# Kernel tuning notes

Hardware: AMD Instinct MI355X
Metric: run time of the kernel (lower is better)

The kernel has to match this reference:

```python
import jax, jax.numpy as jnp
import numpy as np

N_NODES = 100000
N_EDGES = 3200000
N_GRAPHS = 64
NEG_SLOPE = 0.2


def mish(x):
    return x * jnp.tanh(jax.nn.softplus(x))


def gat_layer(x, src, dst, W, b, a_src, a_dst, heads, out_ch, n_nodes):
    # h: [N, H, C]
    h = (x @ W).reshape(n_nodes, heads, out_ch)
    alpha_s = jnp.sum(h * a_src[None], axis=-1)  # [N, H]
    alpha_d = jnp.sum(h * a_dst[None], axis=-1)  # [N, H]
    e = jax.nn.leaky_relu(alpha_s[src] + alpha_d[dst], NEG_SLOPE)  # [E, H]
    # scatter-softmax over incoming edges of each destination node
    emax = jax.ops.segment_max(e, dst, num_segments=n_nodes)  # [N, H]
    ee = jnp.exp(e - emax[dst])
    den = jax.ops.segment_sum(ee, dst, num_segments=n_nodes)
    alpha = ee / (den[dst] + 1e-16)  # [E, H]
    msg = h[src] * alpha[..., None]  # [E, H, C]
    out = jax.ops.segment_sum(msg, dst, num_segments=n_nodes)
    return out.reshape(n_nodes, heads * out_ch) + b


def setup_inputs() -> dict:
    key = jax.random.key(0)
    ks = jax.random.split(key, 10)
    x = jax.random.normal(ks[0], (N_NODES, 128), dtype=jnp.float32)
    edge_index = jax.random.randint(ks[1], (2, N_EDGES), 0, N_NODES, dtype=jnp.int64)
    batch = jnp.sort(jax.random.randint(ks[2], (N_NODES,), 0, N_GRAPHS, dtype=jnp.int64))
    s1 = 1.0 / np.sqrt(128.0)
    s2 = 1.0 / np.sqrt(16.0)
    return {
        "x": x,
        "edge_index": edge_index,
        "batch": batch,
        "W1": jax.random.normal(ks[3], (128, 16), dtype=jnp.float32) * s1,
        "b1": jnp.zeros((16,), dtype=jnp.float32),
        "a_src1": jax.random.normal(ks[4], (4, 4), dtype=jnp.float32) * 0.5,
        "a_dst1": jax.random.normal(ks[5], (4, 4), dtype=jnp.float32) * 0.5,
        "W2": jax.random.normal(ks[6], (16, 32), dtype=jnp.float32) * s2,
        "b2": jnp.zeros((32,), dtype=jnp.float32),
        "a_src2": jax.random.normal(ks[7], (1, 32), dtype=jnp.float32) * 0.5,
        "a_dst2": jax.random.normal(ks[8], (1, 32), dtype=jnp.float32) * 0.5,
    }


def reference(x, edge_index, batch, W1, b1, a_src1, a_dst1, W2, b2, a_src2, a_dst2):
    n = x.shape[0]
    # PyG GATConv default add_self_loops=True
    loop = jnp.arange(n, dtype=edge_index.dtype)
    src = jnp.concatenate([edge_index[0], loop])
    dst = jnp.concatenate([edge_index[1], loop])
    h = mish(gat_layer(x, src, dst, W1, b1, a_src1, a_dst1, heads=4, out_ch=4, n_nodes=n))
    h = mish(gat_layer(h, src, dst, W2, b2, a_src2, a_dst2, heads=1, out_ch=32, n_nodes=n))
    # global_mean_pool
    sums = jax.ops.segment_sum(h, batch, num_segments=N_GRAPHS)
    cnts = jax.ops.segment_sum(jnp.ones((n,), h.dtype), batch, num_segments=N_GRAPHS)
    return sums / jnp.maximum(cnts, 1.0)[:, None]
```

## Files before the change

### kernel.cpp

```cpp
#include <hip/hip_runtime.h>
#include <hip/hip_fp16.h>
#include <math.h>

#define NEG_SLOPE 0.2f
#define GB 192
#define SB 256
#define NBMAX 1024
#define CAP 5120
#define CAPH 2560

typedef _Float16 half2v __attribute__((ext_vector_type(2)));
typedef _Float16 half4v __attribute__((ext_vector_type(4)));

__device__ __forceinline__ float mishf(float x) {
    if (x > 15.f) return x;
    float ex = __expf(x);
    float y = 1.f + ex;
    float y2 = y * y;
    return x * (y2 - 1.f) / (y2 + 1.f);
}

__device__ __forceinline__ float lw(float e) {
    return __expf(fmaxf(e, NEG_SLOPE * e));
}

__device__ __forceinline__ float hdot2a(half2v a, half2v b, float c) {
#if __has_builtin(__builtin_amdgcn_fdot2)
    return __builtin_amdgcn_fdot2(a, b, c, false);
#else
    return (float)a.x * (float)b.x + (float)a.y * (float)b.y + c;
#endif
}

__global__ __launch_bounds__(1024) void front_kernel(
        const float* __restrict__ x, const float* __restrict__ W1,
        const float* __restrict__ a_dst,
        const float* __restrict__ W2, const float* __restrict__ as2,
        const float* __restrict__ ad2,
        _Float16* __restrict__ hpre1h, float* __restrict__ addst,
        float* __restrict__ vs, float* __restrict__ vd,
        const int* __restrict__ src, const int* __restrict__ dst,
        int E, int Etot, int CH, int NB, int N, int NT,
        int* __restrict__ cursor, int* __restrict__ pairs) {
    __shared__ __attribute__((aligned(16))) char smem[42240];
    int tid = threadIdx.x;
    if (blockIdx.x < GB) {
        float* Wlt = (float*)smem;
        float* xs  = Wlt + 16 * 132;
        if (blockIdx.x == 0 && tid < 16) {
            float ps = 0.f, pd = 0.f;
            #pragma unroll
            for (int c = 0; c < 32; c++) {
                float w = W2[tid * 32 + c];
                ps += w * as2[c];
                pd += w * ad2[c];
            }
            vs[tid] = ps; vd[tid] = pd;
        }
        for (int i = tid; i < 2048; i += 1024) Wlt[(i & 15) * 132 + (i >> 4)] = W1[i];
        int nl = tid >> 4, ch = tid & 15;
        for (int t = blockIdx.x; t < NT; t += GB) {
            int nodebase = t * 64;
            int nvalid = min(64, N - nodebase);
            __syncthreads();
            const float4* x4 = (const float4*)(x + (size_t)nodebase * 128);
            #pragma unroll
            for (int u = 0; u < 2; u++) {
                int i = tid + (u << 10);
                int tnl = i >> 5;
                if (tnl < nvalid) {
                    float4 v = x4[i];
                    int k = (i & 31) * 4;
                    float* dp = &xs[tnl * 132 + k];
                    dp[0] = v.x; dp[1] = v.y; dp[2] = v.z; dp[3] = v.w;
                }
            }
            __syncthreads();
            if (nl < nvalid) {
                const float4* xr4 = (const float4*)&xs[nl * 132];
                const float4* wr4 = (const float4*)&Wlt[ch * 132];
                float acc = 0.f;
                #pragma unroll
                for (int k4 = 0; k4 < 32; k4++) {
                    float4 xv = xr4[k4];
                    float4 wv = wr4[k4];
                    acc += xv.x * wv.x + xv.y * wv.y + xv.z * wv.z + xv.w * wv.w;
                }
                int node = nodebase + nl;
                hpre1h[node * 16 + ch] = (_Float16)acc;
                float pd = acc * a_dst[ch];
                pd += __shfl_xor(pd, 1); pd += __shfl_xor(pd, 2);
                if ((ch & 3) == 0) addst[node * 4 + (ch >> 2)] = pd;
            }
        }
    } else {
        int* lcnt  = (int*)smem;
        int* lbase = lcnt + 2 * NBMAX;
        int blk = blockIdx.x - GB;
        int nb2 = 2 * NB;
        for (int b = tid; b < nb2; b += 1024) lcnt[b] = 0;
        __syncthreads();
        int ibeg = blk * CH, iend = min((blk + 1) * CH, Etot);
        int cd[16];
        #pragma unroll
        for (int u = 0; u < 16; u++) {
            int i = ibeg + tid + (u << 10);
            int d = -1;
            if (i < iend) d = (i < E) ? dst[i] : (i - E);
            cd[u] = d;
            if (d >= 0) atomicAdd(&lcnt[d >> 6], 1);
        }
        for (int i = ibeg + (16 << 10) + tid; i < iend; i += 1024) {
            int d = (i < E) ? dst[i] : (i - E);
            atomicAdd(&lcnt[d >> 6], 1);
        }
        __syncthreads();
        for (int b = tid; b < nb2; b += 1024) {
            int h = lcnt[b];
            lbase[b] = h ? atomicAdd(&cursor[b], h) : 0;
        }
        __syncthreads();
        for (int b = tid; b < nb2; b += 1024) lcnt[b] = 0;
        __syncthreads();
        #pragma unroll
        for (int u = 0; u < 16; u++) {
            int i = ibeg + tid + (u << 10);
            int d = cd[u];
            if (d < 0) continue;
            int s = (i < E) ? src[i] : d;
            int idx2 = d >> 6;
            int r = atomicAdd(&lcnt[idx2], 1);
            int pos = lbase[idx2] + r;
            pos = pos < CAPH ? pos : CAPH - 1;
            size_t addr = (size_t)(idx2 >> 1) * CAP + ((idx2 & 1) ? (CAP - 1 - pos) : pos);
            pairs[addr] = s | ((d & 63) << 17);
        }
        for (int i = ibeg + (16 << 10) + tid; i < iend; i += 1024) {
            int d = (i < E) ? dst[i] : (i - E);
            int s = (i < E) ? src[i] : d;
            int idx2 = d >> 6;
            int r = atomicAdd(&lcnt[idx2], 1);
            int pos = lbase[idx2] + r;
            pos = pos < CAPH ? pos : CAPH - 1;
            size_t addr = (size_t)(idx2 >> 1) * CAP + ((idx2 & 1) ? (CAP - 1 - pos) : pos);
            pairs[addr] = s | ((d & 63) << 17);
        }
    }
}

__global__ __launch_bounds__(256) void csragg1_kernel(
        const int* __restrict__ pairs, const int* __restrict__ btotal,
        int NB, int N,
        int* __restrict__ ssorted, int* __restrict__ rs, int* __restrict__ re,
        const float* __restrict__ a_src1, const float* __restrict__ addst,
        const _Float16* __restrict__ hpre1h, const float* __restrict__ b1,
        const float* __restrict__ vs, const float* __restrict__ vd,
        _Float16* __restrict__ hpost1h,
        float* __restrict__ as2n, float* __restrict__ ad2n) {
    __shared__ int deg[64];
    __shared__ int s[64];
    __shared__ int cur[64];
    __shared__ __attribute__((aligned(16))) int lds_sorted[CAPH];
    int tid = threadIdx.x, bh = blockIdx.x;
    int B = bh >> 1, half = bh & 1;
    int nb0 = (B << 7) + (half << 6);
    int cnt_nodes = min(64, N - nb0);
    int c = min(btotal[bh], CAPH);
    int rbase = B * CAP + (half ? CAP - c : 0);
    if (tid < 64) deg[tid] = 0;
    __syncthreads();
    for (int j = tid; j < c; j += 256)
        atomicAdd(&deg[(pairs[rbase + j] >> 17) & 63], 1);
    __syncthreads();
    if (tid < 64) s[tid] = deg[tid];
    __syncthreads();
    for (int o = 1; o < 64; o <<= 1) {
        int v = 0;
        if (tid < 64 && tid >= o) v = s[tid - o];
        __syncthreads();
        if (tid < 64) s[tid] += v;
        __syncthreads();
    }
    if (tid < 64) {
        int ex = s[tid] - deg[tid];
        cur[tid] = ex;
        if (tid < cnt_nodes) {
            rs[nb0 + tid] = bh * CAPH + ex;
            re[nb0 + tid] = bh * CAPH + ex + deg[tid];
        }
    }
    __syncthreads();
    for (int j = tid; j < c; j += 256) {
        int p = pairs[rbase + j];
        int pos = atomicAdd(&cur[(p >> 17) & 63], 1);
        lds_sorted[pos < CAPH ? pos : CAPH - 1] = p & 0x1FFFF;
    }
    __syncthreads();

    {
        int t4 = c >> 2;
        const int4* ls4 = (const int4*)lds_sorted;
        int4* gs4 = (int4*)(ssorted + (size_t)bh * CAPH);
        for (int j = tid; j < t4; j += 256) gs4[j] = ls4[j];
        for (int j = (t4 << 2) + tid; j < c; j += 256)
            ssorted[(size_t)bh * CAPH + j] = lds_sorted[j];
    }

    int wave = tid >> 6;
    int lane = tid & 63;
    int head = lane & 3, er = lane >> 2;
    int c0 = head * 4;
    half2v w01, w23;
    w01.x = (_Float16)a_src1[c0];     w01.y = (_Float16)a_src1[c0 + 1];
    w23.x = (_Float16)a_src1[c0 + 2]; w23.y = (_Float16)a_src1[c0 + 3];
    for (int r = 0; r < 16; r++) {
        int ln = (wave << 4) + r;
        if (ln >= cnt_nodes) break;
        int node = nb0 + ln;
        int end = cur[ln];
        int start = end - deg[ln];
        float adh = addst[node * 4 + head];
        float den = 0.f, a0 = 0.f, a1 = 0.f, a2 = 0.f, a3 = 0.f;
        int last = end - 1;
        int jb = start;
        for (; jb + 16 <= end; jb += 16) {
            int s0 = lds_sorted[jb + er];
            half4v h = *(const half4v*)(hpre1h + (size_t)s0 * 16 + c0);
            half2v hlo = __builtin_shufflevector(h, h, 0, 1);
            half2v hhi = __builtin_shufflevector(h, h, 2, 3);
            float p = hdot2a(hlo, w01, hdot2a(hhi, w23, 0.f));
            float w = lw(p + adh);
            den += w;
            a0 += (float)h.x * w; a1 += (float)h.y * w;
            a2 += (float)h.z * w; a3 += (float)h.w * w;
        }
        if (jb < end) {
            int j0 = jb + er;
            int k0 = (j0 <= last) ? j0 : last;
            int s0 = lds_sorted[k0];
            half4v h = *(const half4v*)(hpre1h + (size_t)s0 * 16 + c0);
            half2v hlo = __builtin_shufflevector(h, h, 0, 1);
            half2v hhi = __builtin_shufflevector(h, h, 2, 3);
            float p = hdot2a(hlo, w01, hdot2a(hhi, w23, 0.f));
            float w = (j0 <= last) ? lw(p + adh) : 0.f;
            den += w;
            a0 += (float)h.x * w; a1 += (float)h.y * w;
            a2 += (float)h.z * w; a3 += (float)h.w * w;
        }
        a0 += __shfl_xor(a0, 4);  a1 += __shfl_xor(a1, 4);  a2 += __shfl_xor(a2, 4);  a3 += __shfl_xor(a3, 4);  den += __shfl_xor(den, 4);
        a0 += __shfl_xor(a0, 8);  a1 += __shfl_xor(a1, 8);  a2 += __shfl_xor(a2, 8);  a3 += __shfl_xor(a3, 8);  den += __shfl_xor(den, 8);
        a0 += __shfl_xor(a0, 16); a1 += __shfl_xor(a1, 16); a2 += __shfl_xor(a2, 16); a3 += __shfl_xor(a3, 16); den += __shfl_xor(den, 16);
        a0 += __shfl_xor(a0, 32); a1 += __shfl_xor(a1, 32); a2 += __shfl_xor(a2, 32); a3 += __shfl_xor(a3, 32); den += __shfl_xor(den, 32);
        if (er == 0) {
            float inv = 1.f / (den + 1e-16f);
            float o0 = mishf(a0 * inv + b1[c0]);
            float o1 = mishf(a1 * inv + b1[c0 + 1]);
            float o2 = mishf(a2 * inv + b1[c0 + 2]);
            float o3 = mishf(a3 * inv + b1[c0 + 3]);
            half4v oh;
            oh.x = (_Float16)o0; oh.y = (_Float16)o1;
            oh.z = (_Float16)o2; oh.w = (_Float16)o3;
            *(half4v*)(hpost1h + (size_t)node * 16 + c0) = oh;
            float ps = o0 * vs[c0] + o1 * vs[c0 + 1] + o2 * vs[c0 + 2] + o3 * vs[c0 + 3];
            float pd = o0 * vd[c0] + o1 * vd[c0 + 1] + o2 * vd[c0 + 2] + o3 * vd[c0 + 3];
            ps += __shfl_xor(ps, 1); pd += __shfl_xor(pd, 1);
            ps += __shfl_xor(ps, 2); pd += __shfl_xor(pd, 2);
            if (head == 0) { as2n[node] = ps; ad2n[node] = pd; }
        }
    }
}

__global__ void agg2_kernel(const int* __restrict__ rs, const int* __restrict__ re,
                            const int* __restrict__ ssorted,
                            const float* __restrict__ as2n, const float* __restrict__ ad2n,
                            const _Float16* __restrict__ hpost1h,
                            float* __restrict__ agg16, float* __restrict__ denv, int N) {
    int wave = threadIdx.x >> 6;
    int lane = threadIdx.x & 63;
    int node = blockIdx.x * 4 + wave;
    if (node >= N) return;
    int start = rs[node], end = re[node];
    int q = lane & 3, er = lane >> 2;
    int c0 = q * 4;
    float adh = ad2n[node];
    const _Float16* hb = hpost1h + c0;
    float den = 0.f, a0 = 0.f, a1 = 0.f, a2 = 0.f, a3 = 0.f;
    int last = end - 1;
    int jb = start;
    for (; jb + 16 <= end; jb += 16) {
        int s0 = __builtin_nontemporal_load(ssorted + jb + er);
        float w = lw(as2n[s0] + adh);
        half4v h = *(const half4v*)(hb + (size_t)s0 * 16);
        den += w;
        a0 += (float)h.x * w; a1 += (float)h.y * w;
        a2 += (float)h.z * w; a3 += (float)h.w * w;
    }
    if (jb < end) {
        int j0 = jb + er;
        int k0 = (j0 <= last) ? j0 : last;
        int s0 = __builtin_nontemporal_load(ssorted + k0);
        float w = (j0 <= last) ? lw(as2n[s0] + adh) : 0.f;
        half4v h = *(const half4v*)(hb + (size_t)s0 * 16);
        den += w;
        a0 += (float)h.x * w; a1 += (float)h.y * w;
        a2 += (float)h.z * w; a3 += (float)h.w * w;
    }
    a0 += __shfl_xor(a0, 4);  a1 += __shfl_xor(a1, 4);  a2 += __shfl_xor(a2, 4);  a3 += __shfl_xor(a3, 4);  den += __shfl_xor(den, 4);
    a0 += __shfl_xor(a0, 8);  a1 += __shfl_xor(a1, 8);  a2 += __shfl_xor(a2, 8);  a3 += __shfl_xor(a3, 8);  den += __shfl_xor(den, 8);
    a0 += __shfl_xor(a0, 16); a1 += __shfl_xor(a1, 16); a2 += __shfl_xor(a2, 16); a3 += __shfl_xor(a3, 16); den += __shfl_xor(den, 16);
    a0 += __shfl_xor(a0, 32); a1 += __shfl_xor(a1, 32); a2 += __shfl_xor(a2, 32); a3 += __shfl_xor(a3, 32); den += __shfl_xor(den, 32);
    if (er == 0) {
        float4 o; o.x = a0; o.y = a1; o.z = a2; o.w = a3;
        *(float4*)(agg16 + (size_t)node * 16 + c0) = o;
        if (q == 0) denv[node] = den;
    }
}

__global__ void post2pool_kernel(const float* __restrict__ agg16, const float* __restrict__ denv,
                                 const float* __restrict__ W2, const float* __restrict__ b2,
                                 const int* __restrict__ batch,
                                 float* __restrict__ pool, float* __restrict__ cnt, int N) {
    __shared__ float Wl[16 * 32];
    int tid = threadIdx.x;
    for (int i = tid; i < 512; i += 256) Wl[i] = W2[i];
    __syncthreads();
    int r = tid >> 5, ch = tid & 31;
    float bc = b2[ch];
    int base = blockIdx.x * 128;
    int cur = -1;
    float sum = 0.f, c = 0.f;
    for (int it = 0; it < 16; it++) {
        int n = base + it * 8 + r;
        if (n >= N) break;
        int g = batch[n];
        if (g != cur) {
            if (cur >= 0) {
                atomicAdd(&pool[cur * 32 + ch], sum);
                if (ch == 0) atomicAdd(&cnt[cur], c);
            }
            cur = g; sum = 0.f; c = 0.f;
        }
        const float* ar = agg16 + (size_t)n * 16;
        float acc = 0.f;
        #pragma unroll
        for (int k = 0; k < 16; k++) acc += ar[k] * Wl[k * 32 + ch];
        float val = mishf(acc / (denv[n] + 1e-16f) + bc);
        sum += val;
        c += 1.f;
    }
    if (cur >= 0) {
        atomicAdd(&pool[cur * 32 + ch], sum);
        if (ch == 0) atomicAdd(&cnt[cur], c);
    }
}

__global__ void fin_kernel(const float* __restrict__ pool, const float* __restrict__ cnt,
                           float* __restrict__ out, int NG) {
    int i = blockIdx.x * blockDim.x + threadIdx.x;
    if (i >= NG * 32) return;
    out[i] = pool[i] / fmaxf(cnt[i >> 5], 1.0f);
}

extern "C" void kernel_launch(void* const* d_in, const int* in_sizes, int n_in,
                              void* d_out, int out_size, void* d_ws, size_t ws_size,
                              hipStream_t stream) {
    const float* x   = (const float*)d_in[0];
    const int* eidx  = (const int*)d_in[1];
    const int* batch = (const int*)d_in[2];
    const float* W1  = (const float*)d_in[3];
    const float* b1  = (const float*)d_in[4];
    const float* as1 = (const float*)d_in[5];
    const float* ad1 = (const float*)d_in[6];
    const float* W2  = (const float*)d_in[7];
    const float* b2  = (const float*)d_in[8];
    const float* as2 = (const float*)d_in[9];
    const float* ad2 = (const float*)d_in[10];
    float* out = (float*)d_out;

    int N = in_sizes[0] / 128;
    int E = in_sizes[1] / 2;
    int Etot = E + N;
    int NG = out_size / 32;
    const int* esrc = eidx;
    const int* edst = eidx + E;

    int NB = (N + 127) >> 7;
    int NBH = NB * 2;
    int NT = (N + 63) >> 6;
    int CH = (Etot + SB - 1) / SB;

    char* p = (char*)d_ws;
    auto alloc = [&](size_t nbytes) {
        p = (char*)(((uintptr_t)p + 15) & ~(uintptr_t)15);
        void* r = (void*)p; p += nbytes; return r;
    };
    int* pairs        = (int*)alloc((size_t)NB * CAP * 4);
    int* ssorted      = (int*)alloc((size_t)NBH * CAPH * 4);
    int* rs           = (int*)alloc((size_t)N * 4);
    int* re           = (int*)alloc((size_t)N * 4);
    int* cursor       = (int*)alloc((size_t)NBH * 4);
    _Float16* hpre1h  = (_Float16*)alloc((size_t)N * 16 * 2);
    _Float16* hpost1h = (_Float16*)alloc((size_t)N * 16 * 2);
    float* addst1  = (float*)alloc((size_t)N * 4 * 4);
    float* as2n    = (float*)alloc((size_t)N * 4);
    float* ad2n    = (float*)alloc((size_t)N * 4);
    float* agg16   = (float*)alloc((size_t)N * 16 * 4);
    float* denv    = (float*)alloc((size_t)N * 4);
    float* vs      = (float*)alloc(16 * 4);
    float* vd      = (float*)alloc(16 * 4);
    float* pool    = (float*)alloc((size_t)NG * 32 * 4);
    float* cnt     = (float*)alloc((size_t)NG * 4);

    hipMemsetAsync(cursor, 0, (size_t)NBH * 4, stream);
    hipMemsetAsync(pool, 0, (size_t)NG * 32 * 4, stream);
    hipMemsetAsync(cnt, 0, (size_t)NG * 4, stream);

    front_kernel<<<GB + SB, 1024, 0, stream>>>(x, W1, ad1, W2, as2, ad2,
                                               hpre1h, addst1, vs, vd,
                                               esrc, edst, E, Etot, CH, NB, N, NT,
                                               cursor, pairs);
    csragg1_kernel<<<NBH, 256, 0, stream>>>(pairs, cursor, NB, N,
                                            ssorted, rs, re, as1, addst1, hpre1h,
                                            b1, vs, vd, hpost1h, as2n, ad2n);
    agg2_kernel<<<(N + 3) / 4, 256, 0, stream>>>(rs, re, ssorted, as2n, ad2n, hpost1h,
                                                 agg16, denv, N);
    post2pool_kernel<<<(N + 127) / 128, 256, 0, stream>>>(agg16, denv, W2, b2, batch,
                                                          pool, cnt, N);
    fin_kernel<<<(NG * 32 + 255) / 256, 256, 0, stream>>>(pool, cnt, out, NG);
}
```

Measured before the change: 330.4 us.

## Stage edge bucketing through LDS for coalesced pair writes

The bucketing blocks now sort their chunk of edges locally in shared memory, using a block-wide prefix scan over bucket counts. They then write the pairs out in bucket order, so global stores become contiguous runs instead of scattered writes. Source indices are loaded once in the first pass and kept in registers rather than re-read. The scatter block count rises to 320 with a smaller per-block chunk, and shared memory grows to about 62KB. The extra scan, the per-element binary search on the write-out and the lower occupancy are added in exchange.

```diff
diff --git a/kernel.cpp b/kernel.cpp
--- a/kernel.cpp
+++ b/kernel.cpp
@@ -4,8 +4,8 @@
 
 #define NEG_SLOPE 0.2f
 #define GB 192
-#define SB 256
-#define NBMAX 1024
+#define SB 320
+#define CHMAX 11264
 #define CAP 5120
 #define CAPH 2560
 
@@ -42,7 +42,7 @@
         const int* __restrict__ src, const int* __restrict__ dst,
         int E, int Etot, int CH, int NB, int N, int NT,
         int* __restrict__ cursor, int* __restrict__ pairs) {
-    __shared__ __attribute__((aligned(16))) char smem[42240];
+    __shared__ __attribute__((aligned(16))) char smem[63824];
     int tid = threadIdx.x;
     if (blockIdx.x < GB) {
         float* Wlt = (float*)smem;
@@ -94,56 +94,79 @@
             }
         }
     } else {
-        int* lcnt  = (int*)smem;
-        int* lbase = lcnt + 2 * NBMAX;
+        int nb2 = 2 * NB;
+        int* A    = (int*)smem;
+        int* Boff = A + nb2;
+        int* C    = Boff + nb2;
+        int* buf  = C + nb2;
         int blk = blockIdx.x - GB;
-        int nb2 = 2 * NB;
-        for (int b = tid; b < nb2; b += 1024) lcnt[b] = 0;
+        for (int b = tid; b < nb2; b += 1024) A[b] = 0;
         __syncthreads();
         int ibeg = blk * CH, iend = min((blk + 1) * CH, Etot);
-        int cd[16];
+        int cdv[11], cs[11];
         #pragma unroll
-        for (int u = 0; u < 16; u++) {
+        for (int u = 0; u < 11; u++) {
             int i = ibeg + tid + (u << 10);
-            int d = -1;
-            if (i < iend) d = (i < E) ? dst[i] : (i - E);
-            cd[u] = d;
-            if (d >= 0) atomicAdd(&lcnt[d >> 6], 1);
-        }
-        for (int i = ibeg + (16 << 10) + tid; i < iend; i += 1024) {
-            int d = (i < E) ? dst[i] : (i - E);
-            atomicAdd(&lcnt[d >> 6], 1);
-        }
-        __syncthreads();
+            int d = -1, s = 0;
+            if (i < iend) {
+                if (i < E) { d = dst[i]; s = src[i]; } else { d = i - E; s = d; }
+                atomicAdd(&A[d >> 6], 1);
+            }
+            cdv[u] = d; cs[u] = s;
+        }
+        for (int i = ibeg + CHMAX + tid; i < iend; i += 1024) {
+            int d, s;
+            if (i < E) { d = dst[i]; s = src[i]; } else { d = i - E; s = d; }
+            int f = d >> 6;
+            int pos = atomicAdd(&cursor[f], 1);
+            pos = pos < CAPH ? pos : CAPH - 1;
+            size_t addr = (size_t)(f >> 1) * CAP + ((f & 1) ? (CAP - 1 - pos) : pos);
+            pairs[addr] = s | ((d & 63) << 17);
+        }
+        __syncthreads();
+        for (int b = tid; b < nb2; b += 1024) Boff[b] = A[b];
+        __syncthreads();
+        for (int o = 1; o < nb2; o <<= 1) {
+            int i1 = tid, i2 = tid + 1024;
+            int v1 = 0, v2 = 0;
+            if (i1 < nb2 && i1 >= o) v1 = Boff[i1 - o];
+            if (i2 < nb2 && i2 >= o) v2 = Boff[i2 - o];
+            __syncthreads();
+            if (i1 < nb2) Boff[i1] += v1;
+            if (i2 < nb2) Boff[i2] += v2;
+            __syncthreads();
+        }
         for (int b = tid; b < nb2; b += 1024) {
-            int h = lcnt[b];
-            lbase[b] = h ? atomicAdd(&cursor[b], h) : 0;
-        }
-        __syncthreads();
-        for (int b = tid; b < nb2; b += 1024) lcnt[b] = 0;
+            int cnt = A[b];
+            Boff[b] -= cnt;
+            C[b] = cnt ? atomicAdd(&cursor[b], cnt) : 0;
+        }
+        __syncthreads();
+        for (int b = tid; b < nb2; b += 1024) A[b] = 0;
         __syncthreads();
         #pragma unroll
-        for (int u = 0; u < 16; u++) {
-            int i = ibeg + tid + (u << 10);
-            int d = cd[u];
+        for (int u = 0; u < 11; u++) {
+            int d = cdv[u];
             if (d < 0) continue;
-            int s = (i < E) ? src[i] : d;
-            int idx2 = d >> 6;
-            int r = atomicAdd(&lcnt[idx2], 1);
-            int pos = lbase[idx2] + r;
+            int f = d >> 6;
+            int r = atomicAdd(&A[f], 1);
+            buf[Boff[f] + r] = cs[u] | ((d & 63) << 17);
+        }
+        __syncthreads();
+        int total = iend - ibeg;
+        if (total > CHMAX) total = CHMAX;
+        if (total < 0) total = 0;
+        for (int j = tid; j < total; j += 1024) {
+            int lo = 0, hi = nb2 - 1;
+            while (lo < hi) {
+                int mid = (lo + hi + 1) >> 1;
+                if (Boff[mid] <= j) lo = mid; else hi = mid - 1;
+            }
+            int f = lo;
+            int pos = C[f] + (j - Boff[f]);
             pos = pos < CAPH ? pos : CAPH - 1;
-            size_t addr = (size_t)(idx2 >> 1) * CAP + ((idx2 & 1) ? (CAP - 1 - pos) : pos);
-            pairs[addr] = s | ((d & 63) << 17);
-        }
-        for (int i = ibeg + (16 << 10) + tid; i < iend; i += 1024) {
-            int d = (i < E) ? dst[i] : (i - E);
-            int s = (i < E) ? src[i] : d;
-            int idx2 = d >> 6;
-            int r = atomicAdd(&lcnt[idx2], 1);
-            int pos = lbase[idx2] + r;
-            pos = pos < CAPH ? pos : CAPH - 1;
-            size_t addr = (size_t)(idx2 >> 1) * CAP + ((idx2 & 1) ? (CAP - 1 - pos) : pos);
-            pairs[addr] = s | ((d & 63) << 17);
+            size_t addr = (size_t)(f >> 1) * CAP + ((f & 1) ? (CAP - 1 - pos) : pos);
+            pairs[addr] = buf[j];
         }
     }
 }
```

Measured after the change: 332.9 us. No clear change (+0.7%).
